# Performance work log

Hardware: AMD Instinct MI355X
Metric: run time of the kernel (lower is better)

The kernel has to match this reference:

```python
import jax, jax.numpy as jnp
import numpy as np

N_HEAD = 8
TANH_CLIP = 10.0
NEG = jnp.float32(-1e9)


def setup_inputs() -> dict:
    key = jax.random.key(0)
    ks = jax.random.split(key, 10)
    B, N, E = 128, 1000, 128
    s = lambda k, shape: (jax.random.normal(k, shape, dtype=jnp.float32) * 0.05)
    return dict(
        node_embeddings=s(ks[0], (B, N, E)),
        graph_embedding=s(ks[1], (B, E)),
        Wqkv=s(ks[2], (E, 3 * E)), bqkv=s(ks[3], (3 * E,)),
        Wfix=s(ks[4], (E, E)), bfix=s(ks[5], (E,)),
        Wstep=s(ks[6], (2 * E, E)), bstep=s(ks[7], (E,)),
        Wmlp=s(ks[8], (E, E)), bmlp=s(ks[9], (E,)),
    )


def reference(node_embeddings, graph_embedding, Wqkv, bqkv, Wfix, bfix,
              Wstep, bstep, Wmlp, bmlp):
    B, N, E = node_embeddings.shape
    H = N_HEAD
    d = E // H
    scale = 1.0 / jnp.sqrt(jnp.float32(d))

    # shared projections (done once, like the torch code)
    qkv = node_embeddings @ Wqkv + bqkv               # [B,N,3E]
    k, v, logit_k = jnp.split(qkv, 3, axis=-1)        # each [B,N,E]
    kh = k.reshape(B, N, H, d).transpose(0, 2, 1, 3)  # [B,H,N,d]
    vh = v.reshape(B, N, H, d).transpose(0, 2, 1, 3)  # [B,H,N,d]
    fixed = graph_embedding @ Wfix + bfix             # [B,E]
    first = node_embeddings[:, 0, :]                  # [B,E]

    init_cur = jnp.zeros((B,), jnp.int32)             # depot = node 0
    init_mask = jnp.zeros((B, N), bool).at[:, 0].set(True)  # True = visited/masked
    batch_idx = jnp.arange(B)

    def step(carry, _):
        cur, mask, total = carry
        last = jnp.take_along_axis(node_embeddings, cur[:, None, None], axis=1)[:, 0, :]  # [B,E]
        q = fixed + jnp.concatenate([first, last], axis=-1) @ Wstep + bstep               # [B,E]
        qh = q.reshape(B, H, d)
        attn = jnp.einsum('bhd,bhnd->bhn', qh, kh) * scale
        attn = jnp.where(mask[:, None, :], NEG, attn)
        attn = jax.nn.softmax(attn, axis=-1)
        ctx = jnp.einsum('bhn,bhnd->bhd', attn, vh).reshape(B, E)
        x = ctx @ Wmlp + bmlp
        logits = jnp.einsum('be,bne->bn', x, logit_k) * scale
        logits = jnp.tanh(logits) * TANH_CLIP
        logits = jnp.where(mask, NEG, logits)
        log_p = jax.nn.log_softmax(logits, axis=-1)
        act = jnp.argmax(log_p, axis=-1).astype(jnp.int32)   # greedy decode
        lp = jnp.take_along_axis(log_p, act[:, None], axis=-1)[:, 0]
        new_mask = mask.at[batch_idx, act].set(True)
        return (act, new_mask, total + lp), act

    (cur, mask, total), seq = jax.lax.scan(
        step, (init_cur, init_mask, jnp.zeros((B,), jnp.float32)), None, length=N - 1)
    # total: summed log-prob of selected tour, [B] (matches _log_p_ in torch code)
    return total
```

## Files before the change

### kernel.cpp

```cpp
#include <hip/hip_runtime.h>
#include <hip/hip_fp16.h>

constexpr int kB = 128;
constexpr int kN = 1000;
constexpr int kE = 128;
constexpr int kH = 8;
constexpr float kFP8Scale = 64.f;
constexpr float kQKScale = 0.25f / 64.f;

typedef _Float16 h2 __attribute__((ext_vector_type(2)));
typedef float f2 __attribute__((ext_vector_type(2)));

__device__ __forceinline__ float fast_tanh(float x) {
  float t = __expf(2.f * x);
  return 1.f - 2.f / (t + 1.f);
}

__device__ __forceinline__ unsigned char enc_fp8(float v) {
  unsigned p = __builtin_amdgcn_cvt_pk_fp8_f32(v, v, 0, false);
  return (unsigned char)(p & 0xFF);
}

__device__ __forceinline__ void dotp(unsigned u, f2 qa, f2 qb, f2& sacc) {
  f2 lo = __builtin_amdgcn_cvt_pk_f32_fp8(u, false);
  f2 hi = __builtin_amdgcn_cvt_pk_f32_fp8(u, true);
  sacc += lo * qa;
  sacc += hi * qb;
}
__device__ __forceinline__ float dot16p(uint4 tq, const f2* q2) {
  f2 s = {0.f, 0.f};
  dotp(tq.x, q2[0], q2[1], s);
  dotp(tq.y, q2[2], q2[3], s);
  dotp(tq.z, q2[4], q2[5], s);
  dotp(tq.w, q2[6], q2[7], s);
  return s.x + s.y;
}
__device__ __forceinline__ void vaccp(unsigned u, f2 hv2, f2& a0, f2& a1) {
  f2 lo = __builtin_amdgcn_cvt_pk_f32_fp8(u, false);
  f2 hi = __builtin_amdgcn_cvt_pk_f32_fp8(u, true);
  a0 += hv2 * lo;
  a1 += hv2 * hi;
}
__device__ __forceinline__ void unpack16(uint4 a, uint4 b, f2* q2) {
  unsigned w[8] = {a.x, a.y, a.z, a.w, b.x, b.y, b.z, b.w};
#pragma unroll
  for (int i = 0; i < 8; ++i) {
    h2 hh = __builtin_bit_cast(h2, w[i]);
    q2[i] = f2{(float)hh.x, (float)hh.y};
  }
}

__device__ __forceinline__ void maxcomb(float& m, int& a, float mo, int ao) {
  bool take = (mo > m) || (mo == m && ao < a);
  m = take ? mo : m;
  a = take ? ao : a;
}

template <int CTRL>
__device__ __forceinline__ float dpp_bcastf(float x) {
  return __builtin_bit_cast(
      float, __builtin_amdgcn_update_dpp(0, __builtin_bit_cast(int, x), CTRL,
                                         0xf, 0xf, true));
}
template <int CTRL>
__device__ __forceinline__ int dpp_bcasti(int x) {
  return __builtin_amdgcn_update_dpp(0, x, CTRL, 0xf, 0xf, true);
}
template <int CTRL>
__device__ __forceinline__ float dpp_addf(float x) {
  return x + dpp_bcastf<CTRL>(x);
}
template <int CTRL>
__device__ __forceinline__ void dpp_maxcomb(float& m, int& a) {
  float mo = dpp_bcastf<CTRL>(m);
  int ao = dpp_bcasti<CTRL>(a);
  maxcomb(m, a, mo, ao);
}

__device__ __forceinline__ void barrier_lds() {
  asm volatile("s_waitcnt lgkmcnt(0)" ::: "memory");
  __builtin_amdgcn_s_barrier();
  asm volatile("" ::: "memory");
}

__global__ __launch_bounds__(384) void qkv_kernel(
    const float* __restrict__ ne, const float* __restrict__ Wqkv,
    const float* __restrict__ bqkv, unsigned char* __restrict__ kq,
    unsigned char* __restrict__ vq, unsigned char* __restrict__ lkq) {
  __shared__ float rows[16 * kE];
  int b = blockIdx.x;
  int n0 = blockIdx.y * 16;
  int ntile = min(16, kN - n0);
  int tid = threadIdx.x;

  for (int idx = tid; idx < ntile * kE; idx += 384)
    rows[idx] = ne[(b * kN + n0) * kE + idx];
  __syncthreads();

  int j = tid;
  float acc[16];
#pragma unroll
  for (int r = 0; r < 16; ++r) acc[r] = 0.f;
  for (int i = 0; i < kE; ++i) {
    float w = Wqkv[i * (3 * kE) + j];
#pragma unroll
    for (int r = 0; r < 16; ++r) acc[r] += rows[r * kE + i] * w;
  }
  float bias = bqkv[j];
  unsigned char* dst;
  int col;
  if (j < kE) { dst = kq; col = j; }
  else if (j < 2 * kE) { dst = vq; col = j - kE; }
  else { dst = lkq; col = j - 2 * kE; }
  for (int r = 0; r < ntile; ++r)
    dst[(size_t)(b * kN + n0 + r) * kE + col] =
        enc_fp8((acc[r] + bias) * kFP8Scale);
}

__global__ __launch_bounds__(128) void qbase_kernel(
    const float* __restrict__ ne, const float* __restrict__ ge,
    const float* __restrict__ Wfix, const float* __restrict__ bfix,
    const float* __restrict__ Wstep, const float* __restrict__ bstep,
    float* __restrict__ qbase) {
  __shared__ float g[kE], f[kE];
  int b = blockIdx.x, e = threadIdx.x;
  g[e] = ge[b * kE + e];
  f[e] = ne[(size_t)b * kN * kE + e];
  __syncthreads();
  float acc = bfix[e] + bstep[e];
  for (int i = 0; i < kE; ++i)
    acc += g[i] * Wfix[i * kE + e] + f[i] * Wstep[i * kE + e];
  qbase[b * kE + e] = acc;
}

__global__ __launch_bounds__(128) void qstep_kernel(
    const float* __restrict__ ne, const float* __restrict__ Wstep,
    const float* __restrict__ qbase, __half* __restrict__ qstep) {
  __shared__ float rows[8 * kE];
  int b = blockIdx.x;
  int n0 = blockIdx.y * 8;
  int tid = threadIdx.x;
  const float* Wbot = Wstep + kE * kE;

  for (int idx = tid; idx < 8 * kE; idx += 128)
    rows[idx] = ne[((size_t)b * kN + n0) * kE + idx];
  __syncthreads();

  float acc[8];
#pragma unroll
  for (int r = 0; r < 8; ++r) acc[r] = 0.f;
  for (int i = 0; i < kE; ++i) {
    float w = Wbot[i * kE + tid];
#pragma unroll
    for (int r = 0; r < 8; ++r) acc[r] += rows[r * kE + i] * w;
  }
  float qb = qbase[b * kE + tid];
#pragma unroll
  for (int r = 0; r < 8; ++r)
    qstep[((size_t)b * kN + n0 + r) * kE + tid] =
        __float2half((qb + acc[r]) * kQKScale);
}

__global__ __launch_bounds__(1024) void rollout_kernel(
    const float* __restrict__ Wmlp, const float* __restrict__ bmlp,
    const unsigned char* __restrict__ kq, const unsigned char* __restrict__ vq,
    const unsigned char* __restrict__ lkq, const __half* __restrict__ qstep,
    float* __restrict__ out) {
  __shared__ __align__(16) int rem[1024];
  __shared__ __align__(16) float parts[kE][65];
  __shared__ __align__(16) float wmT[kE][140];
  __shared__ float bm[kE];
  __shared__ __align__(16) float ctx[kE];
  __shared__ __align__(16) __half xh[kE];
  __shared__ float redSum[16][kH];
  __shared__ __align__(16) float4 redPack[16];

  int b = blockIdx.x;
  int tid = threadIdx.x;
  int lane = tid & 63;
  int wave = tid >> 6;
  int g = tid >> 3;
  int t = tid & 7;

  const unsigned char* kqb = kq + (size_t)b * kN * kE;
  const unsigned char* vqb = vq + (size_t)b * kN * kE;
  const unsigned char* lqb = lkq + (size_t)b * kN * kE;
  const __half* qsb = qstep + (size_t)b * kN * kE;

#pragma unroll
  for (int m = 0; m < 16; ++m) {
    int idx = tid * 16 + m;
    wmT[idx & 127][idx >> 7] = Wmlp[idx];
  }
  rem[tid] = (tid < kN - 1) ? tid + 1 : kN - 1;
  if (tid < kE) bm[tid] = bmlp[tid];

  int A = 0;
  uint4 qa, qb_;
  {
    const uint4* qr = (const uint4*)qsb;
    qa = qr[2 * t];
    qb_ = qr[2 * t + 1];
  }
  float total = 0.f;

  int jn[8];
#pragma unroll
  for (int r = 0; r < 8; ++r) {
    int j = g + 128 * r;
    jn[r] = (j < kN - 1) ? j + 1 : -1;
  }

  barrier_lds();

  for (int step = 0; step < kN - 1; ++step) {
    int R = kN - 1 - step;

    uint4 kb0, vb0, kb1, vb1;
    if (jn[0] >= 0) {
      kb0 = ((const uint4*)(kqb + (size_t)jn[0] * kE))[t];
      vb0 = ((const uint4*)(vqb + (size_t)jn[0] * kE))[t];
    }
    if (jn[1] >= 0) {
      kb1 = ((const uint4*)(kqb + (size_t)jn[1] * kE))[t];
      vb1 = ((const uint4*)(vqb + (size_t)jn[1] * kE))[t];
    }
    f2 q2[8];
    unpack16(qa, qb_, q2);
    f2 acc2[8];
#pragma unroll
    for (int i = 0; i < 8; ++i) acc2[i] = f2{0.f, 0.f};
    float den = 0.f;
#pragma unroll
    for (int r = 0; r < 8; ++r) {
      if (jn[r] < 0) break;
      uint4 kk = (r & 1) ? kb1 : kb0;
      uint4 vv = (r & 1) ? vb1 : vb0;
      if (r + 2 < 8 && jn[r + 2] >= 0) {
        if (r & 1) {
          kb1 = ((const uint4*)(kqb + (size_t)jn[r + 2] * kE))[t];
          vb1 = ((const uint4*)(vqb + (size_t)jn[r + 2] * kE))[t];
        } else {
          kb0 = ((const uint4*)(kqb + (size_t)jn[r + 2] * kE))[t];
          vb0 = ((const uint4*)(vqb + (size_t)jn[r + 2] * kE))[t];
        }
      }
      float s = dot16p(kk, q2);
      float hv = __expf(s);
      den += hv;
      f2 hv2 = {hv, hv};
      vaccp(vv.x, hv2, acc2[0], acc2[1]);
      vaccp(vv.y, hv2, acc2[2], acc2[3]);
      vaccp(vv.z, hv2, acc2[4], acc2[5]);
      vaccp(vv.w, hv2, acc2[6], acc2[7]);
    }
    uint4 lu[8];
#pragma unroll
    for (int r = 0; r < 8; ++r)
      if (jn[r] >= 0) lu[r] = ((const uint4*)(lqb + (size_t)jn[r] * kE))[t];
    den = dpp_addf<0x128>(den);
    den += __shfl_xor(den, 16);
    den += __shfl_xor(den, 32);
    if (lane < kH) redSum[wave][lane] = den;
    {
      float av[16];
#pragma unroll
      for (int c = 0; c < 4; ++c) {
        av[4 * c + 0] = acc2[2 * c].x;
        av[4 * c + 1] = acc2[2 * c].y;
        av[4 * c + 2] = acc2[2 * c + 1].x;
        av[4 * c + 3] = acc2[2 * c + 1].y;
      }
#pragma unroll
      for (int i = 0; i < 16; ++i) av[i] = dpp_addf<0x128>(av[i]);
      if (((lane >> 3) & 1) == 0) {
        int chunk = wave * 4 + (lane >> 4);
#pragma unroll
        for (int i = 0; i < 16; ++i)
          parts[t * 16 + i][(chunk + 4 * t) & 63] = av[i];
      }
    }
    barrier_lds();

    {
      int e = tid >> 3, k = tid & 7, hh = e >> 4;
      float s = 0.f;
#pragma unroll
      for (int m = 0; m < 8; ++m)
        s += parts[e][((8 * k + m) + 4 * hh) & 63];
      float d = redSum[2 * k][hh] + redSum[2 * k + 1][hh];
      s = dpp_addf<0xB1>(s);
      s = dpp_addf<0x4E>(s);
      s = dpp_addf<0x141>(s);
      d = dpp_addf<0xB1>(d);
      d = dpp_addf<0x4E>(d);
      d = dpp_addf<0x141>(d);
      if (k == 0) ctx[e] = s / (d * kFP8Scale);
    }
    barrier_lds();

    {
      float xacc = 0.f;
      const float4* c4 = (const float4*)(ctx + t * 16);
      const float4* w4 = (const float4*)(&wmT[g][t * 16]);
#pragma unroll
      for (int k4 = 0; k4 < 4; ++k4) {
        float4 cv = c4[k4];
        float4 wv = w4[k4];
        xacc += cv.x * wv.x + cv.y * wv.y + cv.z * wv.z + cv.w * wv.w;
      }
      xacc = dpp_addf<0xB1>(xacc);
      xacc = dpp_addf<0x4E>(xacc);
      xacc = dpp_addf<0x141>(xacc);
      if (t == 0) xh[g] = __float2half((bm[g] + xacc) * kQKScale);
    }
    barrier_lds();

    int myv = rem[tid];
    int nxt = rem[(tid < 1023) ? tid + 1 : 1023];
    int pra[8], prb[8];
#pragma unroll
    for (int r = 0; r < 8; ++r) {
      int j = g + 128 * r;
      pra[r] = rem[j];
      prb[r] = rem[(j < 1023) ? j + 1 : 1023];
    }
    float m0 = -1e30f;
    int arg = 0x7fffffff;
    {
      f2 x2[8];
      uint4 xv0 = ((const uint4*)xh)[2 * t];
      uint4 xv1 = ((const uint4*)xh)[2 * t + 1];
      unpack16(xv0, xv1, x2);
#pragma unroll
      for (int r = 0; r < 8; ++r)
        if (jn[r] >= 0) {
          float s = dot16p(lu[r], x2);
          s = dpp_addf<0xB1>(s);
          s = dpp_addf<0x4E>(s);
          s = dpp_addf<0x141>(s);
          if (t == r) {
            m0 = fast_tanh(s) * 10.f;
            arg = jn[r];
          }
        }
    }
    float M = m0;
    int argM = arg;
    dpp_maxcomb<0xB1>(M, argM);
    dpp_maxcomb<0x4E>(M, argM);
    dpp_maxcomb<0x141>(M, argM);
    dpp_maxcomb<0x128>(M, argM);
#pragma unroll
    for (int off = 16; off <= 32; off <<= 1) {
      float mo = __shfl_xor(M, off);
      int ao = __shfl_xor(argM, off);
      maxcomb(M, argM, mo, ao);
    }
    float ex = __expf(m0 - M);
    ex = dpp_addf<0xB1>(ex);
    ex = dpp_addf<0x4E>(ex);
    ex = dpp_addf<0x141>(ex);
    ex = dpp_addf<0x128>(ex);
    ex += __shfl_xor(ex, 16);
    ex += __shfl_xor(ex, 32);
    if (lane == 0)
      redPack[wave] = make_float4(M, ex, __int_as_float(argM), 0.f);
    barrier_lds();

    {
      float4 rp = redPack[lane & 15];
      float mw = rp.x, sw = rp.y;
      int aw = __float_as_int(rp.z);
      float Mf = mw;
      int Af = aw;
      dpp_maxcomb<0xB1>(Mf, Af);
      dpp_maxcomb<0x4E>(Mf, Af);
      dpp_maxcomb<0x141>(Mf, Af);
      dpp_maxcomb<0x128>(Mf, Af);
      float sc = sw * __expf(mw - Mf);
      sc = dpp_addf<0xB1>(sc);
      sc = dpp_addf<0x4E>(sc);
      sc = dpp_addf<0x141>(sc);
      sc = dpp_addf<0x128>(sc);
      A = Af;
      total += -logf(sc);
      const uint4* qr = (const uint4*)(qsb + (size_t)A * kE);
      qa = qr[2 * t];
      qb_ = qr[2 * t + 1];
      int Rn = R - 1;
#pragma unroll
      for (int r = 0; r < 8; ++r) {
        int j = g + 128 * r;
        jn[r] = (j < Rn) ? ((pra[r] < A) ? pra[r] : prb[r]) : -1;
      }
      if (tid < R - 1 && myv >= A) rem[tid] = nxt;
    }
  }
  if (tid == 0) out[b] = total;
}

extern "C" void kernel_launch(void* const* d_in, const int* in_sizes, int n_in,
                              void* d_out, int out_size, void* d_ws,
                              size_t ws_size, hipStream_t stream) {
  const float* ne = (const float*)d_in[0];
  const float* ge = (const float*)d_in[1];
  const float* Wqkv = (const float*)d_in[2];
  const float* bqkv = (const float*)d_in[3];
  const float* Wfix = (const float*)d_in[4];
  const float* bfix = (const float*)d_in[5];
  const float* Wstep = (const float*)d_in[6];
  const float* bstep = (const float*)d_in[7];
  const float* Wmlp = (const float*)d_in[8];
  const float* bmlp = (const float*)d_in[9];
  float* out = (float*)d_out;

  size_t nkv = (size_t)kB * kN * kE;
  unsigned char* kq = (unsigned char*)d_ws;
  unsigned char* vq = kq + nkv;
  unsigned char* lkq = vq + nkv;
  __half* qstep = (__half*)(lkq + nkv);
  float* qbase = (float*)(qstep + nkv);

  qkv_kernel<<<dim3(kB, (kN + 15) / 16), 384, 0, stream>>>(ne, Wqkv, bqkv, kq,
                                                           vq, lkq);
  qbase_kernel<<<kB, kE, 0, stream>>>(ne, ge, Wfix, bfix, Wstep, bstep, qbase);
  qstep_kernel<<<dim3(kB, kN / 8), 128, 0, stream>>>(ne, Wstep, qbase, qstep);
  rollout_kernel<<<kB, 1024, 0, stream>>>(Wmlp, bmlp, kq, vq, lkq, qstep, out);
}
```

Before: 8.684 ms.

## Pack context partials and MLP weights as fp16 and track remaining indices in registers

The partial context sums and the Wmlp weights are now stored in LDS as packed fp16 pairs, so the ctx@Wmlp product runs on fdot2 and uses less LDS space and bandwidth. The context reduction is reorganised with a new thread mapping and an extra DPP step. The per-step remaining-node list is kept partly in registers (jn and jn2), so each step reads one value from the rem array instead of two per row. Rounding ctx and the weights to fp16 adds precision error to the logits and could change which node argmax picks.

New measurement: 11.61 ms. +33.7%, slower.

```diff
diff --git a/kernel.cpp b/kernel.cpp
--- a/kernel.cpp
+++ b/kernel.cpp
@@ -10,6 +10,10 @@
 
 typedef _Float16 h2 __attribute__((ext_vector_type(2)));
 typedef float f2 __attribute__((ext_vector_type(2)));
+
+__device__ __forceinline__ h2 pkrtz(float a, float b) {
+  return __builtin_bit_cast(h2, __builtin_amdgcn_cvt_pkrtz(a, b));
+}
 
 __device__ __forceinline__ float fast_tanh(float x) {
   float t = __expf(2.f * x);
@@ -48,6 +52,10 @@
     h2 hh = __builtin_bit_cast(h2, w[i]);
     q2[i] = f2{(float)hh.x, (float)hh.y};
   }
+}
+__device__ __forceinline__ f2 up2(unsigned u) {
+  h2 hh = __builtin_bit_cast(h2, u);
+  return f2{(float)hh.x, (float)hh.y};
 }
 
 __device__ __forceinline__ void maxcomb(float& m, int& a, float mo, int ao) {
@@ -167,10 +175,10 @@
     const unsigned char* __restrict__ lkq, const __half* __restrict__ qstep,
     float* __restrict__ out) {
   __shared__ __align__(16) int rem[1024];
-  __shared__ __align__(16) float parts[kE][65];
-  __shared__ __align__(16) float wmT[kE][140];
+  __shared__ __align__(16) unsigned parts_p[64][66];
+  __shared__ __align__(16) unsigned wm_p[kE][76];
+  __shared__ __align__(16) unsigned ctx_p[64];
   __shared__ float bm[kE];
-  __shared__ __align__(16) float ctx[kE];
   __shared__ __align__(16) __half xh[kE];
   __shared__ float redSum[16][kH];
   __shared__ __align__(16) float4 redPack[16];
@@ -187,10 +195,14 @@
   const unsigned char* lqb = lkq + (size_t)b * kN * kE;
   const __half* qsb = qstep + (size_t)b * kN * kE;
 
-#pragma unroll
-  for (int m = 0; m < 16; ++m) {
-    int idx = tid * 16 + m;
-    wmT[idx & 127][idx >> 7] = Wmlp[idx];
+  {
+    int gg = tid >> 3, q = tid & 7;
+#pragma unroll
+    for (int m = 0; m < 8; ++m) {
+      int w = q * 8 + m;
+      h2 pk = pkrtz(Wmlp[(2 * w) * kE + gg], Wmlp[(2 * w + 1) * kE + gg]);
+      wm_p[gg][w] = __builtin_bit_cast(unsigned, pk);
+    }
   }
   rem[tid] = (tid < kN - 1) ? tid + 1 : kN - 1;
   if (tid < kE) bm[tid] = bmlp[tid];
@@ -204,11 +216,12 @@
   }
   float total = 0.f;
 
-  int jn[8];
+  int jn[8], jn2[8];
 #pragma unroll
   for (int r = 0; r < 8; ++r) {
     int j = g + 128 * r;
     jn[r] = (j < kN - 1) ? j + 1 : -1;
+    jn2[r] = (j + 1 < kN - 1) ? j + 2 : kN - 1;
   }
 
   barrier_lds();
@@ -276,39 +289,48 @@
       if (((lane >> 3) & 1) == 0) {
         int chunk = wave * 4 + (lane >> 4);
 #pragma unroll
-        for (int i = 0; i < 16; ++i)
-          parts[t * 16 + i][(chunk + 4 * t) & 63] = av[i];
+        for (int i2 = 0; i2 < 8; ++i2) {
+          h2 pk = pkrtz(av[2 * i2], av[2 * i2 + 1]);
+          parts_p[i2 * 8 + t][chunk] = __builtin_bit_cast(unsigned, pk);
+        }
       }
     }
     barrier_lds();
 
     {
-      int e = tid >> 3, k = tid & 7, hh = e >> 4;
-      float s = 0.f;
-#pragma unroll
-      for (int m = 0; m < 8; ++m)
-        s += parts[e][((8 * k + m) + 4 * hh) & 63];
-      float d = redSum[2 * k][hh] + redSum[2 * k + 1][hh];
-      s = dpp_addf<0xB1>(s);
-      s = dpp_addf<0x4E>(s);
-      s = dpp_addf<0x141>(s);
-      d = dpp_addf<0xB1>(d);
-      d = dpp_addf<0x4E>(d);
-      d = dpp_addf<0x141>(d);
-      if (k == 0) ctx[e] = s / (d * kFP8Scale);
+      int rho = tid >> 4;
+      int cg = tid & 15;
+      int h = rho & 7;
+      uint2 u01 = *(const uint2*)&parts_p[rho][4 * cg];
+      uint2 u23 = *(const uint2*)&parts_p[rho][4 * cg + 2];
+      f2 s = up2(u01.x) + up2(u01.y) + up2(u23.x) + up2(u23.y);
+      float d = redSum[cg][h];
+      float sx = s.x, sy = s.y;
+      sx = dpp_addf<0xB1>(sx); sy = dpp_addf<0xB1>(sy); d = dpp_addf<0xB1>(d);
+      sx = dpp_addf<0x4E>(sx); sy = dpp_addf<0x4E>(sy); d = dpp_addf<0x4E>(d);
+      sx = dpp_addf<0x141>(sx); sy = dpp_addf<0x141>(sy); d = dpp_addf<0x141>(d);
+      sx = dpp_addf<0x128>(sx); sy = dpp_addf<0x128>(sy); d = dpp_addf<0x128>(d);
+      if (cg == 0) {
+        float inv = 1.f / (d * kFP8Scale);
+        int p = h * 8 + (rho >> 3);
+        ctx_p[p] = __builtin_bit_cast(unsigned, pkrtz(sx * inv, sy * inv));
+      }
     }
     barrier_lds();
 
     {
+      uint4 c0 = ((const uint4*)ctx_p)[2 * t];
+      uint4 c1 = ((const uint4*)ctx_p)[2 * t + 1];
+      uint4 w0 = *(const uint4*)&wm_p[g][8 * t];
+      uint4 w1 = *(const uint4*)&wm_p[g][8 * t + 4];
+      unsigned cw[8] = {c0.x, c0.y, c0.z, c0.w, c1.x, c1.y, c1.z, c1.w};
+      unsigned ww[8] = {w0.x, w0.y, w0.z, w0.w, w1.x, w1.y, w1.z, w1.w};
       float xacc = 0.f;
-      const float4* c4 = (const float4*)(ctx + t * 16);
-      const float4* w4 = (const float4*)(&wmT[g][t * 16]);
-#pragma unroll
-      for (int k4 = 0; k4 < 4; ++k4) {
-        float4 cv = c4[k4];
-        float4 wv = w4[k4];
-        xacc += cv.x * wv.x + cv.y * wv.y + cv.z * wv.z + cv.w * wv.w;
-      }
+#pragma unroll
+      for (int k = 0; k < 8; ++k)
+        xacc = __builtin_amdgcn_fdot2(__builtin_bit_cast(h2, cw[k]),
+                                      __builtin_bit_cast(h2, ww[k]), xacc,
+                                      false);
       xacc = dpp_addf<0xB1>(xacc);
       xacc = dpp_addf<0x4E>(xacc);
       xacc = dpp_addf<0x141>(xacc);
@@ -318,12 +340,11 @@
 
     int myv = rem[tid];
     int nxt = rem[(tid < 1023) ? tid + 1 : 1023];
-    int pra[8], prb[8];
+    int rr2[8];
 #pragma unroll
     for (int r = 0; r < 8; ++r) {
-      int j = g + 128 * r;
-      pra[r] = rem[j];
-      prb[r] = rem[(j < 1023) ? j + 1 : 1023];
+      int j2 = g + 128 * r + 2;
+      rr2[r] = rem[(j2 < 1024) ? j2 : 1023];
     }
     float m0 = -1e30f;
     int arg = 0x7fffffff;
@@ -392,7 +413,9 @@
 #pragma unroll
       for (int r = 0; r < 8; ++r) {
         int j = g + 128 * r;
-        jn[r] = (j < Rn) ? ((pra[r] < A) ? pra[r] : prb[r]) : -1;
+        int nj = (jn[r] < A) ? jn[r] : jn2[r];
+        jn[r] = (j < Rn) ? nj : -1;
+        jn2[r] = (jn2[r] < A) ? jn2[r] : rr2[r];
       }
       if (tid < R - 1 && myv >= A) rem[tid] = nxt;
     }
```
